# Kernel optimization log

Hardware: AMD Instinct MI355X
Metric: run time of the kernel (lower is better)

Reference implementation:

```python
import jax, jax.numpy as jnp
import numpy as np

B, N, D_IN, HID = 8, 2048, 256, 64  # batch, nodes, input hidden, graph hidden (heads=1)
NEG_INF = -9e15  # matches -9000000000000000.0 in the torch code


def setup_inputs() -> dict:
    key = jax.random.key(0)
    k1, k2, k3, k4 = jax.random.split(key, 4)
    node_features = jax.random.normal(k1, (B, N, D_IN), dtype=jnp.float32)
    adj = jax.random.randint(k2, (B, N, N), 0, 2, dtype=jnp.int32)
    W = jax.random.normal(k3, (D_IN, HID), dtype=jnp.float32) / np.sqrt(D_IN).astype(np.float32)
    a = jax.random.normal(k4, (2 * HID, 1), dtype=jnp.float32) * 0.1
    return {"node_features": node_features, "adj": adj, "W": W, "a": a}


def reference(node_features, adj, W, a):
    # Wh = W(node_features): (B, N, HID)
    Wh = jnp.einsum('bnd,dh->bnh', node_features, W)
    a1 = a[:HID, 0]   # attention vector for the 'source' half of the concat
    a2 = a[HID:, 0]   # attention vector for the 'neighbor' half
    f1 = Wh @ a1      # (B, N) = Wh_i . a1
    f2 = Wh @ a2      # (B, N) = Wh_j . a2
    # e_ij = leakyrelu([Wh_i || Wh_j] . a) -- avoids the O(N^2 * 2*HID) concat
    e = jax.nn.leaky_relu(f1[:, :, None] + f2[:, None, :], negative_slope=0.2)  # (B, N, N)
    att = jnp.where(adj > 0, e, jnp.float32(NEG_INF))
    att = jax.nn.softmax(att, axis=2)
    # dropout is identity in eval / with graph_dropout=0.0
    h_prime = jnp.einsum('bij,bjh->bih', att, Wh)  # (B, N, HID)
    return h_prime
```

## Files before the change

### kernel.cpp

```cpp
#include <hip/hip_runtime.h>

#define NB 8
#define NN 2048
#define DIN 256
#define HID 64
#define JSPLIT 4

typedef __bf16 bf16x8_t __attribute__((ext_vector_type(8)));
typedef float f32x16_t __attribute__((ext_vector_type(16)));

__global__ __launch_bounds__(256) void k_wh(
    const float* __restrict__ x, const float* __restrict__ W,
    const float* __restrict__ a,
    __bf16* __restrict__ wht_hi, __bf16* __restrict__ wht_lo,
    float* __restrict__ f1, float* __restrict__ f2)
{
    __shared__ float smem[DIN * 64];
    const int t = threadIdx.x;
    const int g0 = blockIdx.x * 64;
    const int b = g0 >> 11;
    const int n0 = g0 & (NN - 1);

    const float4* x4 = (const float4*)x;
#pragma unroll
    for (int it = 0; it < 16; ++it) {
        int c = t + it * 256;
        int row = c & 63;
        int dg = c >> 6;
        float4 v = x4[(size_t)(g0 + row) * 64 + dg];
        smem[(dg * 4 + 0) * 64 + row] = v.x;
        smem[(dg * 4 + 1) * 64 + row] = v.y;
        smem[(dg * 4 + 2) * 64 + row] = v.z;
        smem[(dg * 4 + 3) * 64 + row] = v.w;
    }
    __syncthreads();

    const int hq = t & 15;
    const int rg = t >> 4;
    const float4* W4 = (const float4*)W;
    float acc[4][4] = {};
#pragma unroll 8
    for (int d = 0; d < DIN; ++d) {
        float4 wv = W4[d * 16 + hq];
        float4 xv = *(const float4*)&smem[d * 64 + rg * 4];
        float xr[4] = {xv.x, xv.y, xv.z, xv.w};
        float wk[4] = {wv.x, wv.y, wv.z, wv.w};
#pragma unroll
        for (int r = 0; r < 4; ++r)
#pragma unroll
            for (int k = 0; k < 4; ++k) acc[r][k] += xr[r] * wk[k];
    }

    float4 a1v = ((const float4*)a)[hq];
    float4 a2v = ((const float4*)a)[16 + hq];
#pragma unroll
    for (int r = 0; r < 4; ++r) {
        float p1 = acc[r][0] * a1v.x + acc[r][1] * a1v.y + acc[r][2] * a1v.z + acc[r][3] * a1v.w;
        float p2 = acc[r][0] * a2v.x + acc[r][1] * a2v.y + acc[r][2] * a2v.z + acc[r][3] * a2v.w;
#pragma unroll
        for (int m = 1; m < 16; m <<= 1) {
            p1 += __shfl_xor(p1, m);
            p2 += __shfl_xor(p2, m);
        }
        if (hq == 0) {
            f1[g0 + rg * 4 + r] = p1;
            f2[g0 + rg * 4 + r] = p2;
        }
    }

    __syncthreads();
#pragma unroll
    for (int r = 0; r < 4; ++r)
#pragma unroll
        for (int k = 0; k < 4; ++k) {
            int h = hq * 4 + k;
            int row = rg * 4 + r;
            smem[h * 64 + (((row >> 2) ^ (h & 15)) << 2) + (row & 3)] = acc[r][k];
        }
    __syncthreads();

    const int h = t >> 2;
    const int rc = t & 3;
    union { __bf16 bh[16]; uint4 u4[2]; } uh, ul;
#pragma unroll
    for (int q = 0; q < 4; ++q) {
        float4 v = *(const float4*)&smem[h * 64 + (((rc * 4 + q) ^ (h & 15)) << 2)];
        float vv[4] = {v.x, v.y, v.z, v.w};
#pragma unroll
        for (int e = 0; e < 4; ++e) {
            float val = vv[e];
            __bf16 hi = (__bf16)val;
            __bf16 lo = (__bf16)(val - (float)hi);
            uh.bh[q * 4 + e] = hi;
            ul.bh[q * 4 + e] = lo;
        }
    }
    size_t obase = (size_t)(b * HID + h) * NN + n0 + rc * 16;
    *(uint4*)&wht_hi[obase] = uh.u4[0];
    *(uint4*)&wht_hi[obase + 8] = uh.u4[1];
    *(uint4*)&wht_lo[obase] = ul.u4[0];
    *(uint4*)&wht_lo[obase + 8] = ul.u4[1];
}

__global__ __launch_bounds__(256) void k_f2max(
    const float* __restrict__ f2, float* __restrict__ f2mx)
{
    __shared__ float red[4];
    const int b = blockIdx.x, t = threadIdx.x;
    float m = -3.4e38f;
    for (int i = t; i < NN; i += 256) m = fmaxf(m, f2[b * NN + i]);
#pragma unroll
    for (int s = 1; s < 64; s <<= 1) m = fmaxf(m, __shfl_xor(m, s));
    if ((t & 63) == 0) red[t >> 6] = m;
    __syncthreads();
    if (t == 0) f2mx[b] = fmaxf(fmaxf(red[0], red[1]), fmaxf(red[2], red[3]));
}

__global__ __launch_bounds__(256) void k_attn(
    const int* __restrict__ adj, const __bf16* __restrict__ wht_hi,
    const __bf16* __restrict__ wht_lo, const float* __restrict__ f1,
    const float* __restrict__ f2, const float* __restrict__ f2mx,
    float* __restrict__ accp, float* __restrict__ zp)
{
    __shared__ __bf16 whi[64 * 128];
    __shared__ __bf16 wlo[64 * 128];
    const int t = threadIdx.x;
    const int w = t >> 6, lane = t & 63;
    const int bx = blockIdx.x;
    const int js = bx & 3;
    const int it = (bx >> 2) & 15;
    const int b = bx >> 6;
    const int I0 = it * 128 + w * 32;
    const int half = lane >> 5;
    const int m32 = lane & 31;
    const int row = I0 + m32;

    const float f1v = f1[b * NN + row];
    float Mi = f1v + f2mx[b];
    Mi = Mi > 0.f ? Mi : 0.2f * Mi;
    const int* adjrow = adj + (size_t)(b * NN + row) * NN;

    f32x16_t acc0, acc1;
#pragma unroll
    for (int i = 0; i < 16; ++i) { acc0[i] = 0.f; acc1[i] = 0.f; }
    float zacc = 0.f;
    const int jb0 = js * 512;

    for (int stg = 0; stg < 4; ++stg) {
        const int jt = jb0 + stg * 128;
        __syncthreads();
#pragma unroll
        for (int cc = 0; cc < 4; ++cc) {
            int c = t + cc * 256;
            int h = c >> 4, g = c & 15;
            int gp = g ^ (h & 15);
            size_t src = (size_t)(b * HID + h) * NN + jt + g * 8;
            *(uint4*)&whi[h * 128 + gp * 8] = *(const uint4*)&wht_hi[src];
            *(uint4*)&wlo[h * 128 + gp * 8] = *(const uint4*)&wht_lo[src];
        }
        __syncthreads();
#pragma unroll
        for (int s = 0; s < 8; ++s) {
            const int jl = jt + s * 16 + half * 8;
            int4 aa = *(const int4*)&adjrow[jl];
            int4 ab = *(const int4*)&adjrow[jl + 4];
            float4 fa = *(const float4*)&f2[b * NN + jl];
            float4 fb = *(const float4*)&f2[b * NN + jl + 4];
            int av[8] = {aa.x, aa.y, aa.z, aa.w, ab.x, ab.y, ab.z, ab.w};
            float fv[8] = {fa.x, fa.y, fa.z, fa.w, fb.x, fb.y, fb.z, fb.w};
            bf16x8_t ahi, alo;
#pragma unroll
            for (int jj = 0; jj < 8; ++jj) {
                float t1 = f1v + fv[jj];
                t1 = t1 > 0.f ? t1 : 0.2f * t1;
                float pv = av[jj] > 0 ? exp2f((t1 - Mi) * 1.4426950408889634f) : 0.f;
                zacc += pv;
                __bf16 hb = (__bf16)pv;
                ahi[jj] = hb;
                alo[jj] = (__bf16)(pv - (float)hb);
            }
            const int gb = 2 * s + half;
            const int gx = gb ^ (m32 & 15);
            bf16x8_t bh0 = *(const bf16x8_t*)&whi[m32 * 128 + (gx << 3)];
            bf16x8_t bl0 = *(const bf16x8_t*)&wlo[m32 * 128 + (gx << 3)];
            bf16x8_t bh1 = *(const bf16x8_t*)&whi[(m32 + 32) * 128 + (gx << 3)];
            bf16x8_t bl1 = *(const bf16x8_t*)&wlo[(m32 + 32) * 128 + (gx << 3)];
            acc0 = __builtin_amdgcn_mfma_f32_32x32x16_bf16(ahi, bh0, acc0, 0, 0, 0);
            acc0 = __builtin_amdgcn_mfma_f32_32x32x16_bf16(ahi, bl0, acc0, 0, 0, 0);
            acc0 = __builtin_amdgcn_mfma_f32_32x32x16_bf16(alo, bh0, acc0, 0, 0, 0);
            acc1 = __builtin_amdgcn_mfma_f32_32x32x16_bf16(ahi, bh1, acc1, 0, 0, 0);
            acc1 = __builtin_amdgcn_mfma_f32_32x32x16_bf16(ahi, bl1, acc1, 0, 0, 0);
            acc1 = __builtin_amdgcn_mfma_f32_32x32x16_bf16(alo, bh1, acc1, 0, 0, 0);
        }
    }

    float zrow = zacc + __shfl_xor(zacc, 32);
    if (lane < 32) zp[(size_t)(js * NB + b) * NN + row] = zrow;
    float* ap = accp + (size_t)(js * NB + b) * NN * HID;
#pragma unroll
    for (int r = 0; r < 16; ++r) {
        int rr = (r & 3) + 8 * (r >> 2) + 4 * half;
        ap[(size_t)(I0 + rr) * HID + m32] = acc0[r];
        ap[(size_t)(I0 + rr) * HID + m32 + 32] = acc1[r];
    }
}

__global__ __launch_bounds__(256) void k_combine(
    const float* __restrict__ accp, const float* __restrict__ zp,
    float* __restrict__ out)
{
    int gid = blockIdx.x * 256 + threadIdx.x;
    int h4 = gid & 15;
    int rowg = gid >> 4;
    float z = 0.f;
    float sx = 0.f, sy = 0.f, sz = 0.f, sw = 0.f;
#pragma unroll
    for (int js = 0; js < JSPLIT; ++js) {
        size_t base = (size_t)js * NB * NN;
        z += zp[base + rowg];
        float4 v = ((const float4*)accp)[(base + rowg) * 16 + h4];
        sx += v.x; sy += v.y; sz += v.z; sw += v.w;
    }
    float zi = 1.f / z;
    float4 o = {sx * zi, sy * zi, sz * zi, sw * zi};
    ((float4*)out)[gid] = o;
}

extern "C" void kernel_launch(void* const* d_in, const int* in_sizes, int n_in,
                              void* d_out, int out_size, void* d_ws, size_t ws_size,
                              hipStream_t stream)
{
    const float* x = (const float*)d_in[0];
    const int* adj = (const int*)d_in[1];
    const float* W = (const float*)d_in[2];
    const float* a = (const float*)d_in[3];
    float* out = (float*)d_out;
    char* ws = (char*)d_ws;

    __bf16* wht_hi = (__bf16*)(ws);
    __bf16* wht_lo = (__bf16*)(ws + (2u << 20));
    float* f1   = (float*)(ws + (4u << 20));
    float* f2   = (float*)(ws + (4u << 20) + (64u << 10));
    float* f2mx = (float*)(ws + (4u << 20) + (128u << 10));
    float* accp = (float*)(ws + (5u << 20));
    float* zp   = (float*)(ws + (21u << 20));

    hipLaunchKernelGGL(k_wh, dim3(256), dim3(256), 0, stream, x, W, a, wht_hi, wht_lo, f1, f2);
    hipLaunchKernelGGL(k_f2max, dim3(NB), dim3(256), 0, stream, f2, f2mx);
    hipLaunchKernelGGL(k_attn, dim3(512), dim3(256), 0, stream, adj, wht_hi, wht_lo, f1, f2, f2mx, accp, zp);
    hipLaunchKernelGGL(k_combine, dim3(1024), dim3(256), 0, stream, accp, zp, out);
}
```

Measured before the change: 259.0 us.

## Drop LDS staging of Wh tiles, load B operands directly, double j-split

The attention kernel no longer stages Wh hi/lo tiles through shared memory with barriers. Each lane now loads its MFMA B fragments straight from global memory, relying on cache. The j dimension is split 8 ways instead of 4, giving 1024 blocks with an occupancy hint, which enlarges the partial accumulator buffer the combine kernel must reduce. It also switches to the hardware exp2 builtin and unrolls the loop. Together these aim to remove barrier stalls and LDS traffic and to raise parallelism, at the cost of more global loads and more partial-sum traffic.

```diff
diff --git a/kernel.cpp b/kernel.cpp
--- a/kernel.cpp
+++ b/kernel.cpp
@@ -4,7 +4,7 @@
 #define NN 2048
 #define DIN 256
 #define HID 64
-#define JSPLIT 4
+#define JSPLIT 8
 
 typedef __bf16 bf16x8_t __attribute__((ext_vector_type(8)));
 typedef float f32x16_t __attribute__((ext_vector_type(16)));
@@ -116,20 +116,18 @@
     if (t == 0) f2mx[b] = fmaxf(fmaxf(red[0], red[1]), fmaxf(red[2], red[3]));
 }
 
-__global__ __launch_bounds__(256) void k_attn(
+__global__ __launch_bounds__(256, 4) void k_attn(
     const int* __restrict__ adj, const __bf16* __restrict__ wht_hi,
     const __bf16* __restrict__ wht_lo, const float* __restrict__ f1,
     const float* __restrict__ f2, const float* __restrict__ f2mx,
     float* __restrict__ accp, float* __restrict__ zp)
 {
-    __shared__ __bf16 whi[64 * 128];
-    __shared__ __bf16 wlo[64 * 128];
     const int t = threadIdx.x;
     const int w = t >> 6, lane = t & 63;
     const int bx = blockIdx.x;
-    const int js = bx & 3;
-    const int it = (bx >> 2) & 15;
-    const int b = bx >> 6;
+    const int js = bx & 7;
+    const int it = (bx >> 3) & 15;
+    const int b = bx >> 7;
     const int I0 = it * 128 + w * 32;
     const int half = lane >> 5;
     const int m32 = lane & 31;
@@ -139,59 +137,50 @@
     float Mi = f1v + f2mx[b];
     Mi = Mi > 0.f ? Mi : 0.2f * Mi;
     const int* adjrow = adj + (size_t)(b * NN + row) * NN;
+    const __bf16* bh0p = wht_hi + (size_t)(b * HID + m32) * NN;
+    const __bf16* bh1p = wht_hi + (size_t)(b * HID + m32 + 32) * NN;
+    const __bf16* bl0p = wht_lo + (size_t)(b * HID + m32) * NN;
+    const __bf16* bl1p = wht_lo + (size_t)(b * HID + m32 + 32) * NN;
+    const float* f2p = f2 + b * NN;
 
     f32x16_t acc0, acc1;
 #pragma unroll
     for (int i = 0; i < 16; ++i) { acc0[i] = 0.f; acc1[i] = 0.f; }
     float zacc = 0.f;
-    const int jb0 = js * 512;
-
-    for (int stg = 0; stg < 4; ++stg) {
-        const int jt = jb0 + stg * 128;
-        __syncthreads();
-#pragma unroll
-        for (int cc = 0; cc < 4; ++cc) {
-            int c = t + cc * 256;
-            int h = c >> 4, g = c & 15;
-            int gp = g ^ (h & 15);
-            size_t src = (size_t)(b * HID + h) * NN + jt + g * 8;
-            *(uint4*)&whi[h * 128 + gp * 8] = *(const uint4*)&wht_hi[src];
-            *(uint4*)&wlo[h * 128 + gp * 8] = *(const uint4*)&wht_lo[src];
-        }
-        __syncthreads();
-#pragma unroll
-        for (int s = 0; s < 8; ++s) {
-            const int jl = jt + s * 16 + half * 8;
-            int4 aa = *(const int4*)&adjrow[jl];
-            int4 ab = *(const int4*)&adjrow[jl + 4];
-            float4 fa = *(const float4*)&f2[b * NN + jl];
-            float4 fb = *(const float4*)&f2[b * NN + jl + 4];
-            int av[8] = {aa.x, aa.y, aa.z, aa.w, ab.x, ab.y, ab.z, ab.w};
-            float fv[8] = {fa.x, fa.y, fa.z, fa.w, fb.x, fb.y, fb.z, fb.w};
-            bf16x8_t ahi, alo;
-#pragma unroll
-            for (int jj = 0; jj < 8; ++jj) {
-                float t1 = f1v + fv[jj];
-                t1 = t1 > 0.f ? t1 : 0.2f * t1;
-                float pv = av[jj] > 0 ? exp2f((t1 - Mi) * 1.4426950408889634f) : 0.f;
-                zacc += pv;
-                __bf16 hb = (__bf16)pv;
-                ahi[jj] = hb;
-                alo[jj] = (__bf16)(pv - (float)hb);
-            }
-            const int gb = 2 * s + half;
-            const int gx = gb ^ (m32 & 15);
-            bf16x8_t bh0 = *(const bf16x8_t*)&whi[m32 * 128 + (gx << 3)];
-            bf16x8_t bl0 = *(const bf16x8_t*)&wlo[m32 * 128 + (gx << 3)];
-            bf16x8_t bh1 = *(const bf16x8_t*)&whi[(m32 + 32) * 128 + (gx << 3)];
-            bf16x8_t bl1 = *(const bf16x8_t*)&wlo[(m32 + 32) * 128 + (gx << 3)];
-            acc0 = __builtin_amdgcn_mfma_f32_32x32x16_bf16(ahi, bh0, acc0, 0, 0, 0);
-            acc0 = __builtin_amdgcn_mfma_f32_32x32x16_bf16(ahi, bl0, acc0, 0, 0, 0);
-            acc0 = __builtin_amdgcn_mfma_f32_32x32x16_bf16(alo, bh0, acc0, 0, 0, 0);
-            acc1 = __builtin_amdgcn_mfma_f32_32x32x16_bf16(ahi, bh1, acc1, 0, 0, 0);
-            acc1 = __builtin_amdgcn_mfma_f32_32x32x16_bf16(ahi, bl1, acc1, 0, 0, 0);
-            acc1 = __builtin_amdgcn_mfma_f32_32x32x16_bf16(alo, bh1, acc1, 0, 0, 0);
-        }
+    const int jb0 = js * 256;
+
+#pragma unroll 4
+    for (int s = 0; s < 16; ++s) {
+        const int jl = jb0 + s * 16 + half * 8;
+        int4 aa = *(const int4*)&adjrow[jl];
+        int4 ab = *(const int4*)&adjrow[jl + 4];
+        float4 fa = *(const float4*)&f2p[jl];
+        float4 fb = *(const float4*)&f2p[jl + 4];
+        bf16x8_t bh0 = *(const bf16x8_t*)&bh0p[jl];
+        bf16x8_t bl0 = *(const bf16x8_t*)&bl0p[jl];
+        bf16x8_t bh1 = *(const bf16x8_t*)&bh1p[jl];
+        bf16x8_t bl1 = *(const bf16x8_t*)&bl1p[jl];
+        int av[8] = {aa.x, aa.y, aa.z, aa.w, ab.x, ab.y, ab.z, ab.w};
+        float fv[8] = {fa.x, fa.y, fa.z, fa.w, fb.x, fb.y, fb.z, fb.w};
+        bf16x8_t ahi, alo;
+#pragma unroll
+        for (int jj = 0; jj < 8; ++jj) {
+            float t1 = f1v + fv[jj];
+            t1 = t1 > 0.f ? t1 : 0.2f * t1;
+            float pv = av[jj] > 0
+                     ? __builtin_amdgcn_exp2f((t1 - Mi) * 1.4426950408889634f)
+                     : 0.f;
+            zacc += pv;
+            __bf16 hb = (__bf16)pv;
+            ahi[jj] = hb;
+            alo[jj] = (__bf16)(pv - (float)hb);
+        }
+        acc0 = __builtin_amdgcn_mfma_f32_32x32x16_bf16(ahi, bh0, acc0, 0, 0, 0);
+        acc0 = __builtin_amdgcn_mfma_f32_32x32x16_bf16(ahi, bl0, acc0, 0, 0, 0);
+        acc0 = __builtin_amdgcn_mfma_f32_32x32x16_bf16(alo, bh0, acc0, 0, 0, 0);
+        acc1 = __builtin_amdgcn_mfma_f32_32x32x16_bf16(ahi, bh1, acc1, 0, 0, 0);
+        acc1 = __builtin_amdgcn_mfma_f32_32x32x16_bf16(ahi, bl1, acc1, 0, 0, 0);
+        acc1 = __builtin_amdgcn_mfma_f32_32x32x16_bf16(alo, bh1, acc1, 0, 0, 0);
     }
 
     float zrow = zacc + __shfl_xor(zacc, 32);
@@ -243,10 +232,10 @@
     float* f2   = (float*)(ws + (4u << 20) + (64u << 10));
     float* f2mx = (float*)(ws + (4u << 20) + (128u << 10));
     float* accp = (float*)(ws + (5u << 20));
-    float* zp   = (float*)(ws + (21u << 20));
+    float* zp   = (float*)(ws + (37u << 20));
 
     hipLaunchKernelGGL(k_wh, dim3(256), dim3(256), 0, stream, x, W, a, wht_hi, wht_lo, f1, f2);
     hipLaunchKernelGGL(k_f2max, dim3(NB), dim3(256), 0, stream, f2, f2mx);
-    hipLaunchKernelGGL(k_attn, dim3(512), dim3(256), 0, stream, adj, wht_hi, wht_lo, f1, f2, f2mx, accp, zp);
+    hipLaunchKernelGGL(k_attn, dim3(1024), dim3(256), 0, stream, adj, wht_hi, wht_lo, f1, f2, f2mx, accp, zp);
     hipLaunchKernelGGL(k_combine, dim3(1024), dim3(256), 0, stream, accp, zp, out);
 }
```

New measurement: 289.5 us. 11.8% more time.

## Preload adjacency as coalesced ballot bitmasks before the attention MFMA loop

Applied to the files above, without the earlier changes.

Before the main loop, each wave reads its 32 rows of adjacency over the block's 512-column slice with coalesced row-wide loads and packs them into per-lane 64-bit masks using ballot. The inner loop then tests bits instead of issuing strided per-row int4 loads. This aims to replace uncoalesced adjacency traffic and its latency with contiguous prefetched reads. It also adds launch bounds with a minimum of 2 blocks, uses the native exp2 intrinsic with an fma-folded exponent, and computes leaky ReLU with fmax. The extra 8 mask registers and the occupancy hint may raise register pressure or cause spills.

```diff
diff --git a/kernel.cpp b/kernel.cpp
--- a/kernel.cpp
+++ b/kernel.cpp
@@ -116,7 +116,7 @@
     if (t == 0) f2mx[b] = fmaxf(fmaxf(red[0], red[1]), fmaxf(red[2], red[3]));
 }
 
-__global__ __launch_bounds__(256) void k_attn(
+__global__ __launch_bounds__(256, 2) void k_attn(
     const int* __restrict__ adj, const __bf16* __restrict__ wht_hi,
     const __bf16* __restrict__ wht_lo, const float* __restrict__ f1,
     const float* __restrict__ f2, const float* __restrict__ f2mx,
@@ -134,17 +134,34 @@
     const int half = lane >> 5;
     const int m32 = lane & 31;
     const int row = I0 + m32;
+    const int jb0 = js * 512;
 
     const float f1v = f1[b * NN + row];
     float Mi = f1v + f2mx[b];
     Mi = Mi > 0.f ? Mi : 0.2f * Mi;
-    const int* adjrow = adj + (size_t)(b * NN + row) * NN;
+    const float LOG2E = 1.4426950408889634f;
+    const float negMiL = -Mi * LOG2E;
+    const float* f2p = f2 + b * NN;
+
+    uint64_t mq[8];
+#pragma unroll
+    for (int k = 0; k < 8; ++k) mq[k] = 0;
+    const int* adjbase = adj + ((size_t)b * NN + I0) * NN + jb0;
+#pragma unroll 4
+    for (int r = 0; r < 32; ++r) {
+        const int* ar = adjbase + (size_t)r * NN;
+        bool keep = (m32 == r);
+#pragma unroll
+        for (int k = 0; k < 8; ++k) {
+            unsigned long long bal = __ballot(ar[k * 64 + lane] != 0);
+            if (keep) mq[k] = bal;
+        }
+    }
 
     f32x16_t acc0, acc1;
 #pragma unroll
     for (int i = 0; i < 16; ++i) { acc0[i] = 0.f; acc1[i] = 0.f; }
     float zacc = 0.f;
-    const int jb0 = js * 512;
 
     for (int stg = 0; stg < 4; ++stg) {
         const int jt = jb0 + stg * 128;
@@ -160,26 +177,27 @@
         }
         __syncthreads();
 #pragma unroll
-        for (int s = 0; s < 8; ++s) {
-            const int jl = jt + s * 16 + half * 8;
-            int4 aa = *(const int4*)&adjrow[jl];
-            int4 ab = *(const int4*)&adjrow[jl + 4];
-            float4 fa = *(const float4*)&f2[b * NN + jl];
-            float4 fb = *(const float4*)&f2[b * NN + jl + 4];
-            int av[8] = {aa.x, aa.y, aa.z, aa.w, ab.x, ab.y, ab.z, ab.w};
+        for (int s8 = 0; s8 < 8; ++s8) {
+            const int jl = jt + s8 * 16 + half * 8;
+            const uint32_t bits8 =
+                (uint32_t)(mq[s8 >> 2] >> (((s8 & 3) * 16) + half * 8)) & 0xffu;
+            float4 fa = *(const float4*)&f2p[jl];
+            float4 fb = *(const float4*)&f2p[jl + 4];
             float fv[8] = {fa.x, fa.y, fa.z, fa.w, fb.x, fb.y, fb.z, fb.w};
             bf16x8_t ahi, alo;
 #pragma unroll
             for (int jj = 0; jj < 8; ++jj) {
                 float t1 = f1v + fv[jj];
-                t1 = t1 > 0.f ? t1 : 0.2f * t1;
-                float pv = av[jj] > 0 ? exp2f((t1 - Mi) * 1.4426950408889634f) : 0.f;
+                t1 = fmaxf(t1, 0.2f * t1);
+                float pv = (bits8 & (1u << jj))
+                         ? __builtin_amdgcn_exp2f(fmaf(t1, LOG2E, negMiL))
+                         : 0.f;
                 zacc += pv;
                 __bf16 hb = (__bf16)pv;
                 ahi[jj] = hb;
                 alo[jj] = (__bf16)(pv - (float)hb);
             }
-            const int gb = 2 * s + half;
+            const int gb = 2 * s8 + half;
             const int gx = gb ^ (m32 & 15);
             bf16x8_t bh0 = *(const bf16x8_t*)&whi[m32 * 128 + (gx << 3)];
             bf16x8_t bl0 = *(const bf16x8_t*)&wlo[m32 * 128 + (gx << 3)];
@@ -192,6 +210,8 @@
             acc1 = __builtin_amdgcn_mfma_f32_32x32x16_bf16(ahi, bl1, acc1, 0, 0, 0);
             acc1 = __builtin_amdgcn_mfma_f32_32x32x16_bf16(alo, bh1, acc1, 0, 0, 0);
         }
+#pragma unroll
+        for (int k = 0; k < 6; ++k) mq[k] = mq[k + 2];
     }
 
     float zrow = zacc + __shfl_xor(zacc, 32);
```

After: 265.8 us. +2.6%, slower.
